# Optimization experiments

Hardware: AMD Instinct MI355X
Metric: run time of the kernel (lower is better)

The kernel has to match this reference:

```python
import jax, jax.numpy as jnp
import numpy as np

B, SQ, SK, D, DV = 2, 1024, 1024, 64, 64
NEG = -1e9


def setup_inputs() -> dict:
    key = jax.random.key(0)
    kq, kk, kv, km = jax.random.split(key, 4)
    return {
        "q": jax.random.normal(kq, (B, SQ, D), dtype=jnp.float32),
        "k": jax.random.normal(kk, (B, SK, D), dtype=jnp.float32),
        "v": jax.random.normal(kv, (B, SK, DV), dtype=jnp.float32),
        "mask": jax.random.randint(km, (B, SK), 0, 2, dtype=jnp.int32),
    }


def reference(q, k, v, mask):
    # L1 (Manhattan) distance scores: [B, Sq, Sk]
    dist = jnp.sum(jnp.abs(q[:, :, None, :] - k[:, None, :, :]), axis=-1)
    scores = -dist
    # mask: [B, Sk] -> broadcast over queries as [B, 1, Sk]
    scores = jnp.where(mask[:, None, :] == 0, NEG, scores)
    attention = jax.nn.softmax(scores, axis=-1)
    # weighted sum of values: [B, Sq, Dv]
    return jnp.einsum("bqk,bkd->bqd", attention, v)
```

## Files before the change

kernel.cpp:

```cpp
#include <hip/hip_runtime.h>
#include <math.h>

#define B_ 2
#define SQ_ 1024
#define SK_ 1024
#define D_ 64
#define DV_ 64
#define QB 4
#define TPB 256
#define NEGC (-1e9f)

__global__ __launch_bounds__(TPB, 4) void manh_attn_kernel(
    const float* __restrict__ qg, const float* __restrict__ kg,
    const float* __restrict__ vg, const int* __restrict__ maskg,
    float* __restrict__ outg) {
  __shared__ float4 qs4[QB * 16];
  __shared__ float4 p4[SK_];
  __shared__ float pv[16][QB][DV_];
  __shared__ float redm[4][QB];
  __shared__ float redl[4][QB];

  const int tid = threadIdx.x;
  const int b = blockIdx.x >> 8;
  const int q0 = (blockIdx.x & 255) * QB;

  ((float*)qs4)[tid] = qg[((size_t)b * SQ_ + q0) * D_ + tid];
  __syncthreads();

  const float4* kb4 = (const float4*)(kg + (size_t)b * SK_ * D_);
  const int* mb = maskg + (size_t)b * SK_;

  int mk[4];
#pragma unroll
  for (int j = 0; j < 4; ++j) mk[j] = mb[tid + 256 * j];

  float dist[4][QB];
#pragma unroll
  for (int j = 0; j < 4; ++j)
#pragma unroll
    for (int qq = 0; qq < QB; ++qq) dist[j][qq] = 0.f;

#pragma unroll 4
  for (int i = 0; i < 16; ++i) {
    float4 k4[4];
#pragma unroll
    for (int j = 0; j < 4; ++j) k4[j] = kb4[(size_t)(tid + 256 * j) * 16 + i];
    float4 q4[QB];
#pragma unroll
    for (int qq = 0; qq < QB; ++qq) q4[qq] = qs4[qq * 16 + i];
#pragma unroll
    for (int j = 0; j < 4; ++j) {
#pragma unroll
      for (int qq = 0; qq < QB; ++qq) {
        dist[j][qq] += fabsf(q4[qq].x - k4[j].x) + fabsf(q4[qq].y - k4[j].y) +
                       fabsf(q4[qq].z - k4[j].z) + fabsf(q4[qq].w - k4[j].w);
      }
    }
  }

  float lmax[QB];
#pragma unroll
  for (int qq = 0; qq < QB; ++qq) lmax[qq] = -INFINITY;
#pragma unroll
  for (int j = 0; j < 4; ++j) {
#pragma unroll
    for (int qq = 0; qq < QB; ++qq) {
      float s = (mk[j] == 0) ? NEGC : -dist[j][qq];
      dist[j][qq] = s;
      lmax[qq] = fmaxf(lmax[qq], s);
    }
  }
#pragma unroll
  for (int off = 32; off > 0; off >>= 1)
#pragma unroll
    for (int qq = 0; qq < QB; ++qq)
      lmax[qq] = fmaxf(lmax[qq], __shfl_down(lmax[qq], off, 64));
  if ((tid & 63) == 0)
#pragma unroll
    for (int qq = 0; qq < QB; ++qq) redm[tid >> 6][qq] = lmax[qq];
  __syncthreads();
  float m[QB];
#pragma unroll
  for (int qq = 0; qq < QB; ++qq)
    m[qq] = fmaxf(fmaxf(redm[0][qq], redm[1][qq]),
                  fmaxf(redm[2][qq], redm[3][qq]));

  float lsum[QB];
#pragma unroll
  for (int qq = 0; qq < QB; ++qq) lsum[qq] = 0.f;
#pragma unroll
  for (int j = 0; j < 4; ++j) {
    float e[QB];
#pragma unroll
    for (int qq = 0; qq < QB; ++qq) {
      e[qq] = __expf(dist[j][qq] - m[qq]);
      lsum[qq] += e[qq];
    }
    p4[tid + 256 * j] = make_float4(e[0], e[1], e[2], e[3]);
  }
#pragma unroll
  for (int off = 32; off > 0; off >>= 1)
#pragma unroll
    for (int qq = 0; qq < QB; ++qq) lsum[qq] += __shfl_down(lsum[qq], off, 64);
  if ((tid & 63) == 0)
#pragma unroll
    for (int qq = 0; qq < QB; ++qq) redl[tid >> 6][qq] = lsum[qq];
  __syncthreads();

  const int col = tid & 15;
  const int chunk = tid >> 4;
  const float4* vb4 = (const float4*)(vg + (size_t)b * SK_ * DV_);
  float4 acc[QB];
#pragma unroll
  for (int qq = 0; qq < QB; ++qq) acc[qq] = make_float4(0.f, 0.f, 0.f, 0.f);

#pragma unroll 4
  for (int t = 0; t < 64; ++t) {
    const int kk = t * 16 + chunk;
    float4 v4 = vb4[(size_t)kk * 16 + col];
    float4 pw = p4[kk];
    acc[0].x += pw.x * v4.x; acc[0].y += pw.x * v4.y;
    acc[0].z += pw.x * v4.z; acc[0].w += pw.x * v4.w;
    acc[1].x += pw.y * v4.x; acc[1].y += pw.y * v4.y;
    acc[1].z += pw.y * v4.z; acc[1].w += pw.y * v4.w;
    acc[2].x += pw.z * v4.x; acc[2].y += pw.z * v4.y;
    acc[2].z += pw.z * v4.z; acc[2].w += pw.z * v4.w;
    acc[3].x += pw.w * v4.x; acc[3].y += pw.w * v4.y;
    acc[3].z += pw.w * v4.z; acc[3].w += pw.w * v4.w;
  }
#pragma unroll
  for (int qq = 0; qq < QB; ++qq)
    ((float4*)&pv[chunk][qq][0])[col] = acc[qq];
  __syncthreads();

  const int qq2 = tid >> 6;
  const int d2 = tid & 63;
  float s = 0.f;
#pragma unroll
  for (int c = 0; c < 16; ++c) s += pv[c][qq2][d2];
  const float linv =
      1.f / (redl[0][qq2] + redl[1][qq2] + redl[2][qq2] + redl[3][qq2]);
  outg[((size_t)b * SQ_ + q0 + qq2) * DV_ + d2] = s * linv;
}

extern "C" void kernel_launch(void* const* d_in, const int* in_sizes, int n_in,
                              void* d_out, int out_size, void* d_ws,
                              size_t ws_size, hipStream_t stream) {
  const float* q = (const float*)d_in[0];
  const float* k = (const float*)d_in[1];
  const float* v = (const float*)d_in[2];
  const int* mask = (const int*)d_in[3];
  float* out = (float*)d_out;
  dim3 grid(B_ * (SQ_ / QB));
  manh_attn_kernel<<<grid, TPB, 0, stream>>>(q, k, v, mask, out);
}
```

Baseline: 85.48 us.

## Split key dimension across blocks with split-softmax combine kernel

Splits the 1024 keys into four tiles processed by separate blocks, each writing a partial output, max and sum to workspace. A second kernel rescales and merges the partials. Within a block, each key row is now read by four threads covering quarter-rows with coalesced loads, and partial distances are reduced with shuffles. This targets more parallelism and better K-load coalescing, at the cost of workspace traffic and an extra kernel launch.

```diff
diff --git a/kernel.cpp b/kernel.cpp
--- a/kernel.cpp
+++ b/kernel.cpp
@@ -8,67 +8,85 @@
 #define DV_ 64
 #define QB 4
 #define TPB 256
+#define KSPLIT 4
+#define KTILE (SK_ / KSPLIT)
 #define NEGC (-1e9f)
 
-__global__ __launch_bounds__(TPB, 4) void manh_attn_kernel(
+__global__ __launch_bounds__(TPB, 4) void manh_attn_part(
     const float* __restrict__ qg, const float* __restrict__ kg,
     const float* __restrict__ vg, const int* __restrict__ maskg,
-    float* __restrict__ outg) {
-  __shared__ float4 qs4[QB * 16];
-  __shared__ float4 p4[SK_];
+    float* __restrict__ ws_o, float* __restrict__ ws_m,
+    float* __restrict__ ws_l) {
+  __shared__ float4 p4[KTILE];
   __shared__ float pv[16][QB][DV_];
   __shared__ float redm[4][QB];
   __shared__ float redl[4][QB];
 
   const int tid = threadIdx.x;
-  const int b = blockIdx.x >> 8;
-  const int q0 = (blockIdx.x & 255) * QB;
-
-  ((float*)qs4)[tid] = qg[((size_t)b * SQ_ + q0) * D_ + tid];
-  __syncthreads();
+  const int split = blockIdx.x & (KSPLIT - 1);
+  const int qgrp = (blockIdx.x >> 2) & 255;
+  const int b = blockIdx.x >> 10;
+  const int q0 = qgrp * QB;
+  const int kbase = split * KTILE;
 
   const float4* kb4 = (const float4*)(kg + (size_t)b * SK_ * D_);
-  const int* mb = maskg + (size_t)b * SK_;
-
-  int mk[4];
-#pragma unroll
-  for (int j = 0; j < 4; ++j) mk[j] = mb[tid + 256 * j];
-
-  float dist[4][QB];
-#pragma unroll
-  for (int j = 0; j < 4; ++j)
-#pragma unroll
-    for (int qq = 0; qq < QB; ++qq) dist[j][qq] = 0.f;
-
-#pragma unroll 4
-  for (int i = 0; i < 16; ++i) {
+  const float4* qrow = (const float4*)(qg + ((size_t)b * SQ_ + q0) * D_);
+  const int* mb = maskg + (size_t)b * SK_ + kbase;
+
+  const int krow = tid >> 2;
+  const int qtr = tid & 3;
+
+  float4 qr[QB][4];
+#pragma unroll
+  for (int qq = 0; qq < QB; ++qq)
+#pragma unroll
+    for (int j = 0; j < 4; ++j) qr[qq][j] = qrow[qq * 16 + (qtr << 2) + j];
+
+  float dall[4][QB];
+#pragma unroll
+  for (int s = 0; s < 4; ++s) {
     float4 k4[4];
 #pragma unroll
-    for (int j = 0; j < 4; ++j) k4[j] = kb4[(size_t)(tid + 256 * j) * 16 + i];
-    float4 q4[QB];
-#pragma unroll
-    for (int qq = 0; qq < QB; ++qq) q4[qq] = qs4[qq * 16 + i];
+    for (int j = 0; j < 4; ++j)
+      k4[j] = kb4[(size_t)(kbase + s * 64 + krow) * 16 + (qtr << 2) + j];
+    float dloc[QB];
+#pragma unroll
+    for (int qq = 0; qq < QB; ++qq) dloc[qq] = 0.f;
 #pragma unroll
     for (int j = 0; j < 4; ++j) {
 #pragma unroll
       for (int qq = 0; qq < QB; ++qq) {
-        dist[j][qq] += fabsf(q4[qq].x - k4[j].x) + fabsf(q4[qq].y - k4[j].y) +
-                       fabsf(q4[qq].z - k4[j].z) + fabsf(q4[qq].w - k4[j].w);
+        float4 a = qr[qq][j];
+        float4 kk = k4[j];
+        dloc[qq] += fabsf(a.x - kk.x) + fabsf(a.y - kk.y) +
+                    fabsf(a.z - kk.z) + fabsf(a.w - kk.w);
       }
     }
-  }
-
-  float lmax[QB];
-#pragma unroll
-  for (int qq = 0; qq < QB; ++qq) lmax[qq] = -INFINITY;
-#pragma unroll
-  for (int j = 0; j < 4; ++j) {
 #pragma unroll
     for (int qq = 0; qq < QB; ++qq) {
-      float s = (mk[j] == 0) ? NEGC : -dist[j][qq];
-      dist[j][qq] = s;
-      lmax[qq] = fmaxf(lmax[qq], s);
+      float t = dloc[qq];
+      t += __shfl_xor(t, 1, 64);
+      t += __shfl_xor(t, 2, 64);
+      dall[s][qq] = t;
     }
+  }
+
+  const int osub = tid & 3;
+  const int okey = osub * 64 + krow;
+  float sc[QB];
+#pragma unroll
+  for (int qq = 0; qq < QB; ++qq) {
+    float t01 = (osub & 1) ? dall[1][qq] : dall[0][qq];
+    float t23 = (osub & 1) ? dall[3][qq] : dall[2][qq];
+    sc[qq] = (osub & 2) ? t23 : t01;
+  }
+  const int mk = mb[okey];
+
+  float s_[QB], lmax[QB];
+#pragma unroll
+  for (int qq = 0; qq < QB; ++qq) {
+    s_[qq] = (mk == 0) ? NEGC : -sc[qq];
+    lmax[qq] = s_[qq];
   }
 #pragma unroll
   for (int off = 32; off > 0; off >>= 1)
@@ -85,19 +103,13 @@
     m[qq] = fmaxf(fmaxf(redm[0][qq], redm[1][qq]),
                   fmaxf(redm[2][qq], redm[3][qq]));
 
-  float lsum[QB];
-#pragma unroll
-  for (int qq = 0; qq < QB; ++qq) lsum[qq] = 0.f;
-#pragma unroll
-  for (int j = 0; j < 4; ++j) {
-    float e[QB];
-#pragma unroll
-    for (int qq = 0; qq < QB; ++qq) {
-      e[qq] = __expf(dist[j][qq] - m[qq]);
-      lsum[qq] += e[qq];
-    }
-    p4[tid + 256 * j] = make_float4(e[0], e[1], e[2], e[3]);
-  }
+  float lsum[QB], e[QB];
+#pragma unroll
+  for (int qq = 0; qq < QB; ++qq) {
+    e[qq] = __expf(s_[qq] - m[qq]);
+    lsum[qq] = e[qq];
+  }
+  p4[okey] = make_float4(e[0], e[1], e[2], e[3]);
 #pragma unroll
   for (int off = 32; off > 0; off >>= 1)
 #pragma unroll
@@ -113,11 +125,10 @@
   float4 acc[QB];
 #pragma unroll
   for (int qq = 0; qq < QB; ++qq) acc[qq] = make_float4(0.f, 0.f, 0.f, 0.f);
-
 #pragma unroll 4
-  for (int t = 0; t < 64; ++t) {
+  for (int t = 0; t < 16; ++t) {
     const int kk = t * 16 + chunk;
-    float4 v4 = vb4[(size_t)kk * 16 + col];
+    float4 v4 = vb4[(size_t)(kbase + kk) * 16 + col];
     float4 pw = p4[kk];
     acc[0].x += pw.x * v4.x; acc[0].y += pw.x * v4.y;
     acc[0].z += pw.x * v4.z; acc[0].w += pw.x * v4.w;
@@ -129,18 +140,46 @@
     acc[3].z += pw.w * v4.z; acc[3].w += pw.w * v4.w;
   }
 #pragma unroll
+  for (int qq = 0; qq < QB; ++qq) ((float4*)&pv[chunk][qq][0])[col] = acc[qq];
+  __syncthreads();
+
+  float lt[QB];
+#pragma unroll
   for (int qq = 0; qq < QB; ++qq)
-    ((float4*)&pv[chunk][qq][0])[col] = acc[qq];
-  __syncthreads();
-
-  const int qq2 = tid >> 6;
+    lt[qq] = redl[0][qq] + redl[1][qq] + redl[2][qq] + redl[3][qq];
+  if (tid < QB) {
+    const size_t row = (size_t)b * SQ_ + q0 + tid;
+    ws_m[row * KSPLIT + split] = m[tid];
+    ws_l[row * KSPLIT + split] = lt[tid];
+  }
+  const int q2 = tid >> 6;
   const int d2 = tid & 63;
-  float s = 0.f;
-#pragma unroll
-  for (int c = 0; c < 16; ++c) s += pv[c][qq2][d2];
-  const float linv =
-      1.f / (redl[0][qq2] + redl[1][qq2] + redl[2][qq2] + redl[3][qq2]);
-  outg[((size_t)b * SQ_ + q0 + qq2) * DV_ + d2] = s * linv;
+  float so = 0.f;
+#pragma unroll
+  for (int c = 0; c < 16; ++c) so += pv[c][q2][d2];
+  const size_t row = (size_t)b * SQ_ + q0 + q2;
+  ws_o[(row * KSPLIT + split) * DV_ + d2] = so;
+}
+
+__global__ __launch_bounds__(TPB) void manh_attn_combine(
+    const float* __restrict__ ws_o, const float* __restrict__ ws_m,
+    const float* __restrict__ ws_l, float* __restrict__ outg) {
+  const int tid = threadIdx.x;
+  const size_t r = (size_t)blockIdx.x * 4 + (tid >> 6);
+  const int d = tid & 63;
+  const float m0 = ws_m[r * 4 + 0], m1 = ws_m[r * 4 + 1];
+  const float m2 = ws_m[r * 4 + 2], m3 = ws_m[r * 4 + 3];
+  const float l0 = ws_l[r * 4 + 0], l1 = ws_l[r * 4 + 1];
+  const float l2 = ws_l[r * 4 + 2], l3 = ws_l[r * 4 + 3];
+  const float gm = fmaxf(fmaxf(m0, m1), fmaxf(m2, m3));
+  const float w0 = __expf(m0 - gm), w1 = __expf(m1 - gm);
+  const float w2 = __expf(m2 - gm), w3 = __expf(m3 - gm);
+  const float L = l0 * w0 + l1 * w1 + l2 * w2 + l3 * w3;
+  const float acc = ws_o[(r * 4 + 0) * DV_ + d] * w0 +
+                    ws_o[(r * 4 + 1) * DV_ + d] * w1 +
+                    ws_o[(r * 4 + 2) * DV_ + d] * w2 +
+                    ws_o[(r * 4 + 3) * DV_ + d] * w3;
+  outg[r * DV_ + d] = acc / L;
 }
 
 extern "C" void kernel_launch(void* const* d_in, const int* in_sizes, int n_in,
@@ -151,6 +190,14 @@
   const float* v = (const float*)d_in[2];
   const int* mask = (const int*)d_in[3];
   float* out = (float*)d_out;
-  dim3 grid(B_ * (SQ_ / QB));
-  manh_attn_kernel<<<grid, TPB, 0, stream>>>(q, k, v, mask, out);
+
+  float* ws = (float*)d_ws;
+  float* ws_o = ws;
+  float* ws_m = ws + (size_t)B_ * SQ_ * KSPLIT * DV_;
+  float* ws_l = ws_m + (size_t)B_ * SQ_ * KSPLIT;
+
+  dim3 grid1(B_ * (SQ_ / QB) * KSPLIT);
+  manh_attn_part<<<grid1, TPB, 0, stream>>>(q, k, v, mask, ws_o, ws_m, ws_l);
+  dim3 grid2(B_ * SQ_ / 4);
+  manh_attn_combine<<<grid2, TPB, 0, stream>>>(ws_o, ws_m, ws_l, out);
 }
```

Measured after the change: 90.94 us. 1.06x slower.
